# Kernel tuning notes

Hardware: AMD Instinct MI355X
Metric: run time of the kernel (lower is better)

## Reference

```python
import jax, jax.numpy as jnp
import numpy as np


def setup_inputs() -> dict:
    key = jax.random.key(0)
    k1, k2 = jax.random.split(key)
    B, Lq, Lk, D = 4, 4096, 4096, 512
    query = jax.random.normal(k1, (B, Lq, D), dtype=jnp.float32)
    value = jax.random.normal(k2, (B, Lk, D), dtype=jnp.float32)
    return {"query": query, "value": value}


def reference(query, value):
    # score: [B, Lq, Lk] = query @ value^T (unscaled, unmasked)
    score = jnp.einsum('bqd,bkd->bqk', query, value)
    attn = jax.nn.softmax(score, axis=-1)
    # context: [B, Lq, D]
    context = jnp.einsum('bqk,bkd->bqd', attn, value)
    return (context, attn)
```

## Files before the change

kernel.cpp:

```cpp
#include <hip/hip_runtime.h>
#include <cstddef>
#include <cstdint>

typedef unsigned short u16;

constexpr int BATCH = 4;
constexpr int Lq = 4096;
constexpr int Lk = 4096;
constexpr int D  = 512;

constexpr int BM = 128, BN = 128, BK = 32;
constexpr int LDA = 40;

using bf16x8 = __attribute__((ext_vector_type(8))) short;
using f32x4  = __attribute__((ext_vector_type(4))) float;

__device__ inline u16 f32_to_bf16_rne(float x) {
    uint32_t u = __builtin_bit_cast(uint32_t, x);
    u += 0x7fff + ((u >> 16) & 1);
    return (u16)(u >> 16);
}
__device__ inline float bf16_bits_to_f32(u16 h) {
    uint32_t u = ((uint32_t)h) << 16;
    return __builtin_bit_cast(float, u);
}
__device__ inline void split2(float x, float y, uint32_t& hi, uint32_t& lo) {
    u16 hx = f32_to_bf16_rne(x);
    u16 hy = f32_to_bf16_rne(y);
    u16 lx = f32_to_bf16_rne(x - bf16_bits_to_f32(hx));
    u16 ly = f32_to_bf16_rne(y - bf16_bits_to_f32(hy));
    hi = (uint32_t)hx | ((uint32_t)hy << 16);
    lo = (uint32_t)lx | ((uint32_t)ly << 16);
}
__device__ inline uint32_t pack2_bf16(float x, float y) {
    return (uint32_t)f32_to_bf16_rne(x) | ((uint32_t)f32_to_bf16_rne(y) << 16);
}
__device__ inline void gld16(const u16* g, u16* l) {
    __builtin_amdgcn_global_load_lds(
        (const __attribute__((address_space(1))) void*)g,
        (__attribute__((address_space(3))) void*)l, 16, 0, 0);
}
__device__ inline f32x4 mfma16(bf16x8 a, bf16x8 b, f32x4 c) {
    return __builtin_amdgcn_mfma_f32_16x16x32_bf16(a, b, c, 0, 0, 0);
}

__global__ __launch_bounds__(256)
void split_bf16(const float* __restrict__ src, u16* __restrict__ hi,
                u16* __restrict__ lo, int n4)
{
    const int i = blockIdx.x * 256 + threadIdx.x;
    if (i >= n4) return;
    const float4 v = ((const float4*)src)[i];
    uint2 h, l;
    split2(v.x, v.y, h.x, l.x);
    split2(v.z, v.w, h.y, l.y);
    ((uint2*)hi)[i] = h;
    ((uint2*)lo)[i] = l;
}

__global__ __launch_bounds__(256)
void transpose_v_bf16(const float* __restrict__ V, u16* __restrict__ VT)
{
    __shared__ float tile[32][33];
    const int b = blockIdx.z;
    const float* in = V + (size_t)b * Lk * D;
    u16* out = VT + (size_t)b * D * Lk;
    const int lk0 = blockIdx.x * 32;
    const int d0  = blockIdx.y * 32;
    const int c  = threadIdx.x & 31;
    const int r0 = threadIdx.x >> 5;
    #pragma unroll
    for (int i = 0; i < 4; ++i) {
        const int r = r0 + 8 * i;
        tile[r][c] = in[(size_t)(lk0 + r) * D + d0 + c];
    }
    __syncthreads();
    #pragma unroll
    for (int i = 0; i < 4; ++i) {
        const int r = r0 + 8 * i;
        out[(size_t)(d0 + r) * Lk + lk0 + c] = f32_to_bf16_rne(tile[c][r]);
    }
}

__global__ __launch_bounds__(512, 2)
void gemm1_8p(const u16* __restrict__ Qhi, const u16* __restrict__ Qlo,
              const u16* __restrict__ Vhi, const u16* __restrict__ Vlo,
              float* __restrict__ Sg)
{
    constexpr int K  = D;
    constexpr int NT = K / 32;
    __shared__ u16 lds[2 * 4 * 8192];

    const int b = blockIdx.z;
    const u16* Ah = Qhi + (size_t)b * Lq * K;
    const u16* Al = Qlo + (size_t)b * Lq * K;
    const u16* Bh = Vhi + (size_t)b * Lk * K;
    const u16* Bl = Vlo + (size_t)b * Lk * K;
    float* C = Sg + (size_t)b * Lq * Lk;

    const int m0 = blockIdx.y * 256;
    const int n0 = blockIdx.x * 256;
    const int t = threadIdx.x, lane = t & 63, w = t >> 6;
    const int wm = (w >> 2) * 128, wn = (w & 3) * 64;
    const int fr = lane & 15, fq = lane >> 4;

    const int cg   = (lane & 3) ^ ((lane >> 3) & 3);
    const int rsub = lane >> 2;
    const int offA0 = (m0 + w * 32 + rsub) * K + cg * 8;
    const int offA1 = offA0 + 16 * K;
    const int offB0 = (n0 + w * 32 + rsub) * K + cg * 8;
    const int offB1 = offB0 + 16 * K;
    const int ch = w * 1024;

    const int swzc = fq ^ ((fr >> 1) & 3);
    const int aRd = (wm + fr) * 64 + swzc * 16;
    const int bRd = (wn + fr) * 64 + swzc * 16;

    f32x4 acc[8][4] = {};
    bf16x8 aH[4], aL[4], bH[4], bL[4];

    {
        u16* a = &lds[ch];
        gld16(Ah + offA0, a);
        gld16(Ah + offA1, a + 512);
        gld16(Al + offA0, a + 8192);
        gld16(Al + offA1, a + 8192 + 512);
        u16* v = &lds[16384 + ch];
        gld16(Bh + offB0, v);
        gld16(Bh + offB1, v + 512);
        gld16(Bl + offB0, v + 8192);
        gld16(Bl + offB1, v + 8192 + 512);
    }
    asm volatile("s_waitcnt vmcnt(0)" ::: "memory");
    __builtin_amdgcn_s_barrier();
    __builtin_amdgcn_sched_barrier(0);

    for (int kt = 0; kt < NT; ++kt) {
        const int cur = kt & 1;
        const char* ls = (const char*)lds + cur * 65536;
        const int kn = (kt + 1) * 32;
        const int nb = (cur ^ 1) * 32768;

        #pragma unroll
        for (int m = 0; m < 4; ++m) {
            aH[m] = *(const bf16x8*)(ls + aRd + m * 1024);
            aL[m] = *(const bf16x8*)(ls + 16384 + aRd + m * 1024);
        }
        #pragma unroll
        for (int n = 0; n < 2; ++n) {
            bH[n] = *(const bf16x8*)(ls + 32768 + bRd + n * 1024);
            bL[n] = *(const bf16x8*)(ls + 49152 + bRd + n * 1024);
        }
        if (kt < NT - 1) {
            u16* a = &lds[nb + ch];
            gld16(Ah + offA0 + kn, a);
            gld16(Ah + offA1 + kn, a + 512);
            gld16(Al + offA0 + kn, a + 8192);
            gld16(Al + offA1 + kn, a + 8192 + 512);
        }
        __builtin_amdgcn_s_barrier();
        asm volatile("s_waitcnt lgkmcnt(0)" ::: "memory");
        __builtin_amdgcn_sched_barrier(0);
        __builtin_amdgcn_s_setprio(1);
        #pragma unroll
        for (int m = 0; m < 4; ++m)
            #pragma unroll
            for (int n = 0; n < 2; ++n) {
                acc[m][n] = mfma16(aH[m], bH[n], acc[m][n]);
                acc[m][n] = mfma16(aH[m], bL[n], acc[m][n]);
                acc[m][n] = mfma16(aL[m], bH[n], acc[m][n]);
            }
        __builtin_amdgcn_s_setprio(0);
        __builtin_amdgcn_s_barrier();
        __builtin_amdgcn_sched_barrier(0);

        #pragma unroll
        for (int n = 2; n < 4; ++n) {
            bH[n] = *(const bf16x8*)(ls + 32768 + bRd + n * 1024);
            bL[n] = *(const bf16x8*)(ls + 49152 + bRd + n * 1024);
        }
        if (kt < NT - 1) {
            u16* v = &lds[nb + 16384 + ch];
            gld16(Bh + offB0 + kn, v);
            gld16(Bh + offB1 + kn, v + 512);
            gld16(Bl + offB0 + kn, v + 8192);
            gld16(Bl + offB1 + kn, v + 8192 + 512);
        }
        __builtin_amdgcn_s_barrier();
        asm volatile("s_waitcnt lgkmcnt(0)" ::: "memory");
        __builtin_amdgcn_sched_barrier(0);
        __builtin_amdgcn_s_setprio(1);
        #pragma unroll
        for (int m = 0; m < 4; ++m)
            #pragma unroll
            for (int n = 2; n < 4; ++n) {
                acc[m][n] = mfma16(aH[m], bH[n], acc[m][n]);
                acc[m][n] = mfma16(aH[m], bL[n], acc[m][n]);
                acc[m][n] = mfma16(aL[m], bH[n], acc[m][n]);
            }
        __builtin_amdgcn_s_setprio(0);
        __builtin_amdgcn_s_barrier();
        __builtin_amdgcn_sched_barrier(0);

        #pragma unroll
        for (int m = 0; m < 4; ++m) {
            aH[m] = *(const bf16x8*)(ls + 4096 + aRd + m * 1024);
            aL[m] = *(const bf16x8*)(ls + 16384 + 4096 + aRd + m * 1024);
        }
        __builtin_amdgcn_s_barrier();
        asm volatile("s_waitcnt lgkmcnt(0)" ::: "memory");
        __builtin_amdgcn_sched_barrier(0);
        __builtin_amdgcn_s_setprio(1);
        #pragma unroll
        for (int m = 0; m < 4; ++m)
            #pragma unroll
            for (int n = 0; n < 2; ++n) {
                acc[4 + m][n] = mfma16(aH[m], bH[n], acc[4 + m][n]);
                acc[4 + m][n] = mfma16(aH[m], bL[n], acc[4 + m][n]);
                acc[4 + m][n] = mfma16(aL[m], bH[n], acc[4 + m][n]);
            }
        __builtin_amdgcn_s_setprio(0);
        __builtin_amdgcn_s_barrier();
        __builtin_amdgcn_sched_barrier(0);

        __builtin_amdgcn_s_setprio(1);
        #pragma unroll
        for (int m = 0; m < 4; ++m)
            #pragma unroll
            for (int n = 2; n < 4; ++n) {
                acc[4 + m][n] = mfma16(aH[m], bH[n], acc[4 + m][n]);
                acc[4 + m][n] = mfma16(aH[m], bL[n], acc[4 + m][n]);
                acc[4 + m][n] = mfma16(aL[m], bH[n], acc[4 + m][n]);
            }
        __builtin_amdgcn_s_setprio(0);
        asm volatile("s_waitcnt vmcnt(0)" ::: "memory");
        __builtin_amdgcn_s_barrier();
        __builtin_amdgcn_sched_barrier(0);
    }

    const int rowb = m0 + wm + fq * 4;
    const int colb = n0 + wn + fr;
    #pragma unroll
    for (int mi = 0; mi < 8; ++mi)
        #pragma unroll
        for (int ni = 0; ni < 4; ++ni)
            #pragma unroll
            for (int r = 0; r < 4; ++r)
                C[(size_t)(rowb + mi * 16 + r) * Lk + colb + ni * 16] = acc[mi][ni][r];
}

__global__ __launch_bounds__(256)
void softmax_inplace(float* __restrict__ S, u16* __restrict__ Pb)
{
    const size_t row = blockIdx.x;
    float* p = S + row * (size_t)Lk;
    const int t = threadIdx.x;

    float4 v[4];
    #pragma unroll
    for (int i = 0; i < 4; ++i) v[i] = ((const float4*)p)[t + i * 256];

    float m = -3.0e38f;
    #pragma unroll
    for (int i = 0; i < 4; ++i)
        m = fmaxf(m, fmaxf(fmaxf(v[i].x, v[i].y), fmaxf(v[i].z, v[i].w)));
    #pragma unroll
    for (int off = 32; off > 0; off >>= 1) m = fmaxf(m, __shfl_xor(m, off));
    __shared__ float redm[4];
    if ((t & 63) == 0) redm[t >> 6] = m;
    __syncthreads();
    m = fmaxf(fmaxf(redm[0], redm[1]), fmaxf(redm[2], redm[3]));

    float s = 0.f;
    #pragma unroll
    for (int i = 0; i < 4; ++i) {
        v[i].x = __expf(v[i].x - m); s += v[i].x;
        v[i].y = __expf(v[i].y - m); s += v[i].y;
        v[i].z = __expf(v[i].z - m); s += v[i].z;
        v[i].w = __expf(v[i].w - m); s += v[i].w;
    }
    #pragma unroll
    for (int off = 32; off > 0; off >>= 1) s += __shfl_xor(s, off);
    __shared__ float reds[4];
    if ((t & 63) == 0) reds[t >> 6] = s;
    __syncthreads();
    s = (reds[0] + reds[1]) + (reds[2] + reds[3]);

    const float inv = 1.0f / s;
    u16* prow = Pb ? Pb + row * (size_t)Lk : nullptr;
    #pragma unroll
    for (int i = 0; i < 4; ++i) {
        v[i].x *= inv; v[i].y *= inv; v[i].z *= inv; v[i].w *= inv;
        ((float4*)p)[t + i * 256] = v[i];
        if (prow) {
            ushort4 h = make_ushort4(f32_to_bf16_rne(v[i].x), f32_to_bf16_rne(v[i].y),
                                     f32_to_bf16_rne(v[i].z), f32_to_bf16_rne(v[i].w));
            ((ushort4*)prow)[t + i * 256] = h;
        }
    }
}

__global__ __launch_bounds__(256, 3)
void gemm2_mfma(const u16* __restrict__ Pg, const u16* __restrict__ VTg,
                float* __restrict__ Cg)
{
    constexpr int K = Lk;
    constexpr int N = D;
    __shared__ u16 sA[BM * BK];
    __shared__ u16 sB[BN * BK];

    const int b = blockIdx.z;
    const u16* A  = Pg  + (size_t)b * Lq * Lk;
    const u16* Bp = VTg + (size_t)b * (size_t)D * Lk;
    float* C = Cg + (size_t)b * Lq * D;

    const int m0 = blockIdx.y * BM;
    const int n0 = blockIdx.x * BN;
    const int t = threadIdx.x, lane = t & 63, wave = t >> 6;
    const int wm = (wave >> 1) * 64, wn = (wave & 1) * 64;
    const int fr = lane & 15, fq = lane >> 4;

    const int r0  = wave * 16 + (lane >> 2);
    const int r1  = r0 + 64;
    const int kc8 = (lane & 3) * 8;
    const int oA0 = (m0 + r0) * K + kc8;
    const int oA1 = (m0 + r1) * K + kc8;
    const int oB0 = (n0 + r0) * K + kc8;
    const int oB1 = (n0 + r1) * K + kc8;
    const int w0 = wave * 512, w1 = (wave + 4) * 512;

    f32x4 acc[4][4] = {};

    for (int k0 = 0; k0 < K; k0 += BK) {
        if (k0) __syncthreads();
        gld16(A  + oA0 + k0, &sA[w0]);
        gld16(A  + oA1 + k0, &sA[w1]);
        gld16(Bp + oB0 + k0, &sB[w0]);
        gld16(Bp + oB1 + k0, &sB[w1]);
        __syncthreads();

        bf16x8 af[4], bf[4];
        #pragma unroll
        for (int x = 0; x < 4; ++x) {
            af[x] = *(const bf16x8*)&sA[(wm + x * 16 + fr) * BK + fq * 8];
            bf[x] = *(const bf16x8*)&sB[(wn + x * 16 + fr) * BK + fq * 8];
        }
        #pragma unroll
        for (int mi = 0; mi < 4; ++mi)
            #pragma unroll
            for (int ni = 0; ni < 4; ++ni)
                acc[mi][ni] = __builtin_amdgcn_mfma_f32_16x16x32_bf16(af[mi], bf[ni], acc[mi][ni], 0, 0, 0);
    }

    #pragma unroll
    for (int mi = 0; mi < 4; ++mi)
        #pragma unroll
        for (int ni = 0; ni < 4; ++ni)
            #pragma unroll
            for (int r = 0; r < 4; ++r) {
                const int row = m0 + wm + mi * 16 + fq * 4 + r;
                const int col = n0 + wn + ni * 16 + fr;
                C[(size_t)row * N + col] = acc[mi][ni][r];
            }
}

__global__ __launch_bounds__(256, 2)
void gemm1_r2(const float* __restrict__ Qg, const float* __restrict__ Vg,
              float* __restrict__ Sg)
{
    constexpr int K = D;
    __shared__ alignas(16) u16 sAhi[BM * LDA];
    __shared__ alignas(16) u16 sAlo[BM * LDA];
    __shared__ alignas(16) u16 sBhi[BN * LDA];
    __shared__ alignas(16) u16 sBlo[BN * LDA];

    const int b = blockIdx.z;
    const float* A  = Qg + (size_t)b * Lq * D;
    const float* Bp = Vg + (size_t)b * Lk * D;
    float* C = Sg + (size_t)b * Lq * Lk;

    const int m0 = blockIdx.y * BM;
    const int n0 = blockIdx.x * BN;
    const int t = threadIdx.x, lane = t & 63, wave = t >> 6;
    const int wm = (wave >> 1) * 64, wn = (wave & 1) * 64;
    const int fr = lane & 15, fq = lane >> 4;
    const int sm = t >> 3, sc = t & 7;

    f32x4 acc[4][4] = {};

    for (int k0 = 0; k0 < K; k0 += BK) {
        if (k0) __syncthreads();
        #pragma unroll
        for (int i = 0; i < 4; ++i) {
            const int m = sm + 32 * i;
            const float4 va = *(const float4*)(A  + (size_t)(m0 + m) * K + k0 + sc * 4);
            const float4 vb = *(const float4*)(Bp + (size_t)(n0 + m) * K + k0 + sc * 4);
            uint2 h, l;
            split2(va.x, va.y, h.x, l.x);
            split2(va.z, va.w, h.y, l.y);
            *(uint2*)&sAhi[m * LDA + sc * 4] = h;
            *(uint2*)&sAlo[m * LDA + sc * 4] = l;
            split2(vb.x, vb.y, h.x, l.x);
            split2(vb.z, vb.w, h.y, l.y);
            *(uint2*)&sBhi[m * LDA + sc * 4] = h;
            *(uint2*)&sBlo[m * LDA + sc * 4] = l;
        }
        __syncthreads();

        bf16x8 ah[4], al[4], bh[4], bl[4];
        #pragma unroll
        for (int x = 0; x < 4; ++x) {
            ah[x] = *(const bf16x8*)&sAhi[(wm + x * 16 + fr) * LDA + fq * 8];
            al[x] = *(const bf16x8*)&sAlo[(wm + x * 16 + fr) * LDA + fq * 8];
            bh[x] = *(const bf16x8*)&sBhi[(wn + x * 16 + fr) * LDA + fq * 8];
            bl[x] = *(const bf16x8*)&sBlo[(wn + x * 16 + fr) * LDA + fq * 8];
        }
        #pragma unroll
        for (int mi = 0; mi < 4; ++mi)
            #pragma unroll
            for (int ni = 0; ni < 4; ++ni) {
                acc[mi][ni] = __builtin_amdgcn_mfma_f32_16x16x32_bf16(ah[mi], bh[ni], acc[mi][ni], 0, 0, 0);
                acc[mi][ni] = __builtin_amdgcn_mfma_f32_16x16x32_bf16(ah[mi], bl[ni], acc[mi][ni], 0, 0, 0);
                acc[mi][ni] = __builtin_amdgcn_mfma_f32_16x16x32_bf16(al[mi], bh[ni], acc[mi][ni], 0, 0, 0);
            }
    }

    #pragma unroll
    for (int mi = 0; mi < 4; ++mi)
        #pragma unroll
        for (int ni = 0; ni < 4; ++ni)
            #pragma unroll
            for (int r = 0; r < 4; ++r) {
                const int row = m0 + wm + mi * 16 + fq * 4 + r;
                const int col = n0 + wn + ni * 16 + fr;
                C[(size_t)row * Lk + col] = acc[mi][ni][r];
            }
}

__global__ __launch_bounds__(256, 2)
void gemm2_r2(const float* __restrict__ Pg, const u16* __restrict__ VTg,
              float* __restrict__ Cg)
{
    constexpr int K = Lk;
    constexpr int N = D;
    __shared__ alignas(16) u16 sA[BM * LDA];
    __shared__ alignas(16) u16 sB[BN * LDA];

    const int b = blockIdx.z;
    const float* A  = Pg  + (size_t)b * Lq * Lk;
    const u16*   Bp = VTg + (size_t)b * (size_t)D * Lk;
    float* C = Cg + (size_t)b * Lq * D;

    const int m0 = blockIdx.y * BM;
    const int n0 = blockIdx.x * BN;
    const int t = threadIdx.x, lane = t & 63, wave = t >> 6;
    const int wm = (wave >> 1) * 64, wn = (wave & 1) * 64;
    const int fr = lane & 15, fq = lane >> 4;
    const int sm = t >> 3, sc = t & 7;
    const int bn = t >> 2, bc = t & 3;

    f32x4 acc[4][4] = {};

    for (int k0 = 0; k0 < K; k0 += BK) {
        if (k0) __syncthreads();
        #pragma unroll
        for (int i = 0; i < 4; ++i) {
            const int m = sm + 32 * i;
            const float4 va = *(const float4*)(A + (size_t)(m0 + m) * K + k0 + sc * 4);
            uint2 h;
            h.x = pack2_bf16(va.x, va.y);
            h.y = pack2_bf16(va.z, va.w);
            *(uint2*)&sA[m * LDA + sc * 4] = h;
        }
        #pragma unroll
        for (int i = 0; i < 2; ++i) {
            const int n = bn + 64 * i;
            const bf16x8 vb = *(const bf16x8*)(Bp + (size_t)(n0 + n) * K + k0 + bc * 8);
            *(bf16x8*)&sB[n * LDA + bc * 8] = vb;
        }
        __syncthreads();

        bf16x8 af[4], bf[4];
        #pragma unroll
        for (int x = 0; x < 4; ++x) {
            af[x] = *(const bf16x8*)&sA[(wm + x * 16 + fr) * LDA + fq * 8];
            bf[x] = *(const bf16x8*)&sB[(wn + x * 16 + fr) * LDA + fq * 8];
        }
        #pragma unroll
        for (int mi = 0; mi < 4; ++mi)
            #pragma unroll
            for (int ni = 0; ni < 4; ++ni)
                acc[mi][ni] = __builtin_amdgcn_mfma_f32_16x16x32_bf16(af[mi], bf[ni], acc[mi][ni], 0, 0, 0);
    }

    #pragma unroll
    for (int mi = 0; mi < 4; ++mi)
        #pragma unroll
        for (int ni = 0; ni < 4; ++ni)
            #pragma unroll
            for (int r = 0; r < 4; ++r) {
                const int row = m0 + wm + mi * 16 + fq * 4 + r;
                const int col = n0 + wn + ni * 16 + fr;
                C[(size_t)row * N + col] = acc[mi][ni][r];
            }
}

extern "C" void kernel_launch(void* const* d_in, const int* in_sizes, int n_in,
                              void* d_out, int out_size, void* d_ws, size_t ws_size,
                              hipStream_t stream)
{
    const float* Q = (const float*)d_in[0];
    const float* V = (const float*)d_in[1];
    float* ctx  = (float*)d_out;
    float* attn = (float*)d_out + (size_t)BATCH * Lq * D;

    constexpr size_t NQ = (size_t)BATCH * Lq * D;
    constexpr size_t NP = (size_t)BATCH * Lq * Lk;
    const size_t need = (5 * NQ + NP) * sizeof(u16);

    if (ws_size >= need) {
        u16* Qhi = (u16*)d_ws;
        u16* Qlo = Qhi + NQ;
        u16* Vhi = Qlo + NQ;
        u16* Vlo = Vhi + NQ;
        u16* VT  = Vlo + NQ;
        u16* Pb  = VT  + NQ;

        const int n4 = (int)(NQ / 4);
        split_bf16<<<dim3(n4 / 256), 256, 0, stream>>>(Q, Qhi, Qlo, n4);
        split_bf16<<<dim3(n4 / 256), 256, 0, stream>>>(V, Vhi, Vlo, n4);
        transpose_v_bf16<<<dim3(Lk / 32, D / 32, BATCH), 256, 0, stream>>>(V, VT);
        gemm1_8p<<<dim3(Lk / 256, Lq / 256, BATCH), 512, 0, stream>>>(Qhi, Qlo, Vhi, Vlo, attn);
        softmax_inplace<<<dim3(BATCH * Lq), 256, 0, stream>>>(attn, Pb);
        gemm2_mfma<<<dim3(D / BN, Lq / BM, BATCH), 256, 0, stream>>>(Pb, VT, ctx);
    } else {
        u16* VT = (u16*)d_ws;
        transpose_v_bf16<<<dim3(Lk / 32, D / 32, BATCH), 256, 0, stream>>>(V, VT);
        gemm1_r2<<<dim3(Lk / BN, Lq / BM, BATCH), 256, 0, stream>>>(Q, V, attn);
        softmax_inplace<<<dim3(BATCH * Lq), 256, 0, stream>>>(attn, nullptr);
        gemm2_r2<<<dim3(D / BN, Lq / BM, BATCH), 256, 0, stream>>>(attn, VT, ctx);
    }
}
```

Before: 740.6 us.

## Fuse partial softmax statistics into QK GEMM epilogue and remap block order

The QK^T GEMM epilogue now computes per-row partial max and exp-sum for each 256-column tile and writes them to workspace. A small kernel combines them into row max and inverse sum, so the softmax pass becomes a single read-exp-write without separate reductions. Both GEMMs also remap block IDs so neighbouring workgroups are spread across the grid, which is meant to improve cache locality. The cost is extra epilogue shuffles and exps, one extra launch, and workspace buffers that reuse the Qhi and Pb regions, which relies on the order of later writes.

```diff
diff --git a/kernel.cpp b/kernel.cpp
--- a/kernel.cpp
+++ b/kernel.cpp
@@ -85,7 +85,8 @@
 __global__ __launch_bounds__(512, 2)
 void gemm1_8p(const u16* __restrict__ Qhi, const u16* __restrict__ Qlo,
               const u16* __restrict__ Vhi, const u16* __restrict__ Vlo,
-              float* __restrict__ Sg)
+              float* __restrict__ Sg, float* __restrict__ Mw,
+              float* __restrict__ Sw)
 {
     constexpr int K  = D;
     constexpr int NT = K / 32;
@@ -98,8 +99,12 @@
     const u16* Bl = Vlo + (size_t)b * Lk * K;
     float* C = Sg + (size_t)b * Lq * Lk;
 
-    const int m0 = blockIdx.y * 256;
-    const int n0 = blockIdx.x * 256;
+    int id = blockIdx.y * 16 + blockIdx.x;
+    id = (id & 7) * 32 + (id >> 3);
+    const int m0 = (id >> 4) * 256;
+    const int n0 = (id & 15) * 256;
+    const int cb = id & 15;
+
     const int t = threadIdx.x, lane = t & 63, w = t >> 6;
     const int wm = (w >> 2) * 128, wn = (w & 3) * 64;
     const int fr = lane & 15, fq = lane >> 4;
@@ -247,6 +252,84 @@
             #pragma unroll
             for (int r = 0; r < 4; ++r)
                 C[(size_t)(rowb + mi * 16 + r) * Lk + colb + ni * 16] = acc[mi][ni][r];
+
+    __syncthreads();
+    float* mxl = (float*)lds;
+    float* sml = mxl + 1024;
+    #pragma unroll
+    for (int mi = 0; mi < 8; ++mi)
+        #pragma unroll
+        for (int r = 0; r < 4; ++r) {
+            float mx = fmaxf(fmaxf(acc[mi][0][r], acc[mi][1][r]),
+                             fmaxf(acc[mi][2][r], acc[mi][3][r]));
+            #pragma unroll
+            for (int off = 1; off < 16; off <<= 1)
+                mx = fmaxf(mx, __shfl_xor(mx, off));
+            float sm = 0.f;
+            #pragma unroll
+            for (int ni = 0; ni < 4; ++ni)
+                sm += __expf(acc[mi][ni][r] - mx);
+            #pragma unroll
+            for (int off = 1; off < 16; off <<= 1)
+                sm += __shfl_xor(sm, off);
+            if (fr == 0) {
+                const int row = wm + mi * 16 + fq * 4 + r;
+                mxl[row * 4 + (w & 3)] = mx;
+                sml[row * 4 + (w & 3)] = sm;
+            }
+        }
+    __syncthreads();
+    if (t < 256) {
+        const float m1 = fmaxf(fmaxf(mxl[t * 4 + 0], mxl[t * 4 + 1]),
+                               fmaxf(mxl[t * 4 + 2], mxl[t * 4 + 3]));
+        float s1 = 0.f;
+        #pragma unroll
+        for (int i = 0; i < 4; ++i)
+            s1 += sml[t * 4 + i] * __expf(mxl[t * 4 + i] - m1);
+        const size_t ix = ((size_t)b * Lq + m0 + t) * 16 + cb;
+        Mw[ix] = m1;
+        Sw[ix] = s1;
+    }
+}
+
+__global__ __launch_bounds__(256)
+void reduce_stats(const float* __restrict__ Mw, const float* __restrict__ Sw,
+                  float* __restrict__ rowM, float* __restrict__ rowI)
+{
+    const int row = blockIdx.x * 256 + threadIdx.x;
+    const float* mp = Mw + (size_t)row * 16;
+    const float* sp = Sw + (size_t)row * 16;
+    float m = mp[0];
+    #pragma unroll
+    for (int i = 1; i < 16; ++i) m = fmaxf(m, mp[i]);
+    float s = 0.f;
+    #pragma unroll
+    for (int i = 0; i < 16; ++i) s += sp[i] * __expf(mp[i] - m);
+    rowM[row] = m;
+    rowI[row] = 1.0f / s;
+}
+
+__global__ __launch_bounds__(256)
+void finalize_softmax(float* __restrict__ S, u16* __restrict__ Pb,
+                      const float* __restrict__ rowM, const float* __restrict__ rowI)
+{
+    const size_t row = blockIdx.x;
+    float* p = S + row * (size_t)Lk;
+    u16* prow = Pb + row * (size_t)Lk;
+    const int t = threadIdx.x;
+    const float m = rowM[row], inv = rowI[row];
+    #pragma unroll
+    for (int i = 0; i < 4; ++i) {
+        float4 v = ((const float4*)p)[t + i * 256];
+        v.x = __expf(v.x - m) * inv;
+        v.y = __expf(v.y - m) * inv;
+        v.z = __expf(v.z - m) * inv;
+        v.w = __expf(v.w - m) * inv;
+        ((float4*)p)[t + i * 256] = v;
+        ushort4 h = make_ushort4(f32_to_bf16_rne(v.x), f32_to_bf16_rne(v.y),
+                                 f32_to_bf16_rne(v.z), f32_to_bf16_rne(v.w));
+        ((ushort4*)prow)[t + i * 256] = h;
+    }
 }
 
 __global__ __launch_bounds__(256)
@@ -314,8 +397,11 @@
     const u16* Bp = VTg + (size_t)b * (size_t)D * Lk;
     float* C = Cg + (size_t)b * Lq * D;
 
-    const int m0 = blockIdx.y * BM;
-    const int n0 = blockIdx.x * BN;
+    int id = blockIdx.y * 4 + blockIdx.x;
+    id = (id & 7) * 16 + (id >> 3);
+    const int m0 = (id >> 2) * BM;
+    const int n0 = (id & 3) * BN;
+
     const int t = threadIdx.x, lane = t & 63, wave = t >> 6;
     const int wm = (wave >> 1) * 64, wn = (wave & 1) * 64;
     const int fr = lane & 15, fq = lane >> 4;
@@ -526,12 +612,18 @@
         u16* VT  = Vlo + NQ;
         u16* Pb  = VT  + NQ;
 
+        float* Mw   = (float*)Pb;
+        float* Sw   = Mw + (size_t)BATCH * Lq * 16;
+        float* rowM = (float*)Qhi;
+        float* rowI = rowM + (size_t)BATCH * Lq;
+
         const int n4 = (int)(NQ / 4);
         split_bf16<<<dim3(n4 / 256), 256, 0, stream>>>(Q, Qhi, Qlo, n4);
         split_bf16<<<dim3(n4 / 256), 256, 0, stream>>>(V, Vhi, Vlo, n4);
         transpose_v_bf16<<<dim3(Lk / 32, D / 32, BATCH), 256, 0, stream>>>(V, VT);
-        gemm1_8p<<<dim3(Lk / 256, Lq / 256, BATCH), 512, 0, stream>>>(Qhi, Qlo, Vhi, Vlo, attn);
-        softmax_inplace<<<dim3(BATCH * Lq), 256, 0, stream>>>(attn, Pb);
+        gemm1_8p<<<dim3(Lk / 256, Lq / 256, BATCH), 512, 0, stream>>>(Qhi, Qlo, Vhi, Vlo, attn, Mw, Sw);
+        reduce_stats<<<dim3(BATCH * Lq / 256), 256, 0, stream>>>(Mw, Sw, rowM, rowI);
+        finalize_softmax<<<dim3(BATCH * Lq), 256, 0, stream>>>(attn, Pb, rowM, rowI);
         gemm2_mfma<<<dim3(D / BN, Lq / BM, BATCH), 256, 0, stream>>>(Pb, VT, ctx);
     } else {
         u16* VT = (u16*)d_ws;
```

New measurement: 781.4 us. +5.5%, slower.
